# Optimization experiments

Hardware: AMD Instinct MI355X
Metric: run time of the kernel (lower is better)

Reference implementation:

```python
import jax, jax.numpy as jnp
import numpy as np

N, D, C, E, K = 100000, 64, 40, 1600000, 2

def setup_inputs() -> dict:
    key = jax.random.key(0)
    k1, k2, k3 = jax.random.split(key, 3)
    x = jax.random.normal(k1, (N, D), dtype=jnp.float32)
    edge_index = jax.random.randint(k2, (2, E), 0, N, dtype=jnp.int64)
    W = jax.random.normal(k3, (D, C), dtype=jnp.float32) * 0.05
    b = jnp.zeros((C,), dtype=jnp.float32)
    return {"x": x, "edge_index": edge_index, "W": W, "b": b}

def reference(x, edge_index, W, b):
    n = x.shape[0]
    self_loop = jnp.arange(n, dtype=edge_index.dtype)
    row = jnp.concatenate([edge_index[0], self_loop])  # [E+N]
    col = jnp.concatenate([edge_index[1], self_loop])  # [E+N]
    # degree over row (out-degree incl. self loops), as in torch_geometric.utils.degree
    deg = jax.ops.segment_sum(jnp.ones_like(row, dtype=x.dtype), row, num_segments=n)
    deg_inv_sqrt = jnp.where(deg > 0, jax.lax.rsqrt(deg), 0.0)
    norm = deg_inv_sqrt[row] * deg_inv_sqrt[col]  # [E+N]
    # K hops of SpMM: out[r] += norm_e * x[c] for each edge e=(r,c)
    for _ in range(K):
        x = jax.ops.segment_sum(norm[:, None] * x[col], row, num_segments=n)
    logits = x @ W + b  # [N, C]
    return jax.nn.log_softmax(logits, axis=1)
```

## Files before the change

kernel.cpp:

```cpp
#include <hip/hip_runtime.h>
#include <math.h>


#define D_FEAT 64
#define NCLS 40
#define BROWS 512
#define BROWS_LOG 9
#define BINCAP 10240
#define CSRCAP 12288
#define EPT 25

typedef float v2f __attribute__((ext_vector_type(2)));

__device__ __forceinline__ unsigned pack_bf16_2(float lo, float hi) {
    unsigned ulo = __float_as_uint(lo);
    unsigned uhi = __float_as_uint(hi);
    ulo = (ulo + 0x7fffu + ((ulo >> 16) & 1u)) >> 16;
    uhi = (uhi + 0x7fffu + ((uhi >> 16) & 1u)) & 0xffff0000u;
    return uhi | ulo;
}

__device__ __forceinline__ void acc2p(unsigned u, v2f& a) {
    v2f v;
    v.x = __uint_as_float(u << 16);
    v.y = __uint_as_float(u & 0xffff0000u);
    a += v;
}

__global__ void zero_cursors_kernel(int* __restrict__ cur, int nb) {
    int i = blockIdx.x * blockDim.x + threadIdx.x;
    if (i < nb) cur[i] = 0;
}

__global__ __launch_bounds__(256) void bin_edges_kernel(const int* __restrict__ rows,
                                                        const int* __restrict__ cols,
                                                        int* __restrict__ bucket_cursor,
                                                        unsigned* __restrict__ bins,
                                                        int e, int nb) {
    __shared__ int cnt[512];
    for (int i = threadIdx.x; i < nb; i += 256) cnt[i] = 0;
    __syncthreads();
    int base = blockIdx.x * (256 * EPT) + threadIdx.x;
    int rr[EPT], cc[EPT];
#pragma unroll
    for (int k = 0; k < EPT; k++) {
        int idx = base + k * 256;
        if (idx < e) { rr[k] = rows[idx]; cc[k] = cols[idx]; }
        else { rr[k] = -1; cc[k] = 0; }
    }
#pragma unroll
    for (int k = 0; k < EPT; k++)
        if (rr[k] >= 0) atomicAdd(&cnt[rr[k] >> BROWS_LOG], 1);
    __syncthreads();
    for (int i = threadIdx.x; i < nb; i += 256) {
        int c = cnt[i];
        cnt[i] = (c > 0) ? atomicAdd(&bucket_cursor[i], c) : 0;
    }
    __syncthreads();
#pragma unroll
    for (int k = 0; k < EPT; k++) {
        if (rr[k] >= 0) {
            int b = rr[k] >> BROWS_LOG;
            int pos = atomicAdd(&cnt[b], 1);
            bins[(size_t)b * BINCAP + pos] =
                ((unsigned)(rr[k] & (BROWS - 1)) << 17) | (unsigned)cc[k];
        }
    }
}

__global__ __launch_bounds__(512) void build_csr_kernel(const unsigned* __restrict__ bins,
                                                        const int* __restrict__ bucket_cursor,
                                                        int* __restrict__ csr_col,
                                                        uint2* __restrict__ row_info,
                                                        float* __restrict__ dis,
                                                        int* __restrict__ perm, int n) {
    __shared__ int cnt[512];
    __shared__ int sm[512];
    __shared__ int cur[512];
    __shared__ int lcsr[CSRCAP];
    int b = blockIdx.x;
    int tid = threadIdx.x;
    int m = bucket_cursor[b];
    cnt[tid] = 0;
    __syncthreads();
    const unsigned* bp = bins + (size_t)b * BINCAP;
    for (int i = tid; i < m; i += 512) atomicAdd(&cnt[bp[i] >> 17], 1);
    __syncthreads();
    int c = cnt[tid];
    int padded = (c + 3) & ~3;
    int r = b * BROWS + tid;
    if (r < n) dis[r] = rsqrtf(1.0f + (float)c);
    sm[tid] = padded;
    __syncthreads();
    for (int off = 1; off < 512; off <<= 1) {
        int t = (tid >= off) ? sm[tid - off] : 0;
        __syncthreads();
        sm[tid] += t;
        __syncthreads();
    }
    int off0 = sm[tid] - padded;
    cur[tid] = off0;
    if (r < n) row_info[r] = make_uint2((unsigned)(b * CSRCAP + off0), (unsigned)padded);
    __syncthreads();
    for (int i = tid; i < m; i += 512) {
        unsigned u = bp[i];
        int pos = atomicAdd(&cur[u >> 17], 1);
        lcsr[pos] = (int)(u & 0x1FFFFu);
    }
    __syncthreads();
    if (r < n) {
        for (int j = c; j < padded; j++) lcsr[off0 + j] = n;
    }
    __syncthreads();
    int tot = sm[511];
    int4* cp4 = (int4*)(csr_col + (size_t)b * CSRCAP);
    const int4* l4 = (const int4*)lcsr;
    for (int i = tid; i < (tot >> 2); i += 512) cp4[i] = l4[i];

    __syncthreads();
    if (tid < 64) cnt[tid] = 0;
    __syncthreads();
    int bin = min(padded >> 2, 63);
    if (r < n) atomicAdd(&cnt[bin], 1);
    __syncthreads();
    if (tid < 64) sm[tid] = cnt[tid];
    __syncthreads();
    for (int off = 1; off < 64; off <<= 1) {
        int t = (tid >= off && tid < 64) ? sm[tid - off] : 0;
        __syncthreads();
        if (tid < 64) sm[tid] += t;
        __syncthreads();
    }
    if (tid < 64) cur[tid] = sm[tid] - cnt[tid];
    __syncthreads();
    if (r < n) {
        int rank = atomicAdd(&cur[bin], 1);
        perm[b * BROWS + rank] = r;
    } else {
        perm[b * BROWS + tid] = -1;
    }
}

__global__ __launch_bounds__(256) void sort_rows_kernel(int* __restrict__ csr_col,
                                                        const uint2* __restrict__ row_info,
                                                        int n) {
    int wid = (int)((blockIdx.x * blockDim.x + threadIdx.x) >> 6);
    int lane = threadIdx.x & 63;
    int r0 = wid * 2, r1 = r0 + 1;
    if (r0 >= n) return;
    uint2 i0 = row_info[r0];
    uint2 i1 = (r1 < n) ? row_info[r1] : make_uint2(0u, 0u);
    int p0 = (int)i0.y, p1 = (int)i1.y;
    if (p0 <= 32 && p1 <= 32) {
        int half = lane >> 5, hl = lane & 31;
        int base = half ? (int)i1.x : (int)i0.x;
        int pad  = half ? p1 : p0;
        int key = (hl < pad) ? csr_col[base + hl] : 0x7fffffff;
#pragma unroll
        for (int k = 2; k <= 32; k <<= 1) {
#pragma unroll
            for (int j = k >> 1; j > 0; j >>= 1) {
                int other = __shfl_xor(key, j, 64);
                bool takeMin = (((hl & j) == 0) == ((hl & k) == 0));
                int mn = min(key, other), mx = max(key, other);
                key = takeMin ? mn : mx;
            }
        }
        if (hl < pad) csr_col[base + hl] = key;
    } else {
        for (int t = 0; t < 2; t++) {
            int base = t ? (int)i1.x : (int)i0.x;
            int pad  = t ? p1 : p0;
            if (pad == 0) continue;
            if (pad <= 64) {
                int key = (lane < pad) ? csr_col[base + lane] : 0x7fffffff;
#pragma unroll
                for (int k = 2; k <= 64; k <<= 1) {
#pragma unroll
                    for (int j = k >> 1; j > 0; j >>= 1) {
                        int other = __shfl_xor(key, j, 64);
                        bool takeMin = (((lane & j) == 0) == ((lane & k) == 0));
                        int mn = min(key, other), mx = max(key, other);
                        key = takeMin ? mn : mx;
                    }
                }
                if (lane < pad) csr_col[base + lane] = key;
            } else if (lane == 0) {
                for (int i2 = 1; i2 < pad; i2++) {
                    int kk = csr_col[base + i2];
                    int j2 = i2 - 1;
                    while (j2 >= 0 && csr_col[base + j2] > kk) {
                        csr_col[base + j2 + 1] = csr_col[base + j2]; j2--;
                    }
                    csr_col[base + j2 + 1] = kk;
                }
            }
        }
    }
}

__global__ void scale_x_kernel(const float* __restrict__ x, const float* __restrict__ dis,
                               unsigned* __restrict__ xs0, unsigned* __restrict__ xs1, int n) {
    int i = blockIdx.x * blockDim.x + threadIdx.x;
    int total = (n + 1) * (D_FEAT / 2);
    if (i >= total) return;
    int node = i >> 5;
    if (node < n) {
        float s = dis[node];
        float2 v = ((const float2*)x)[i];
        xs0[i] = pack_bf16_2(s * v.x, s * v.y);
    } else {
        xs0[i] = 0u;
        xs1[i] = 0u;
    }
}

#define GATHER16(cp, xs_in, ql, base, len)                                  \
    uint2 u0 = make_uint2(0u, 0u), u1 = u0, u2 = u0, u3 = u0;               \
    uint2 u4 = u0, u5 = u0, u6 = u0, u7 = u0;                               \
    uint2 u8 = u0, u9 = u0, u10 = u0, u11 = u0;                             \
    uint2 u12 = u0, u13 = u0, u14 = u0, u15 = u0;                           \
    if (base < len) {                                                       \
        uint4 cv = cp[(base >> 2) + 0];                                     \
        u0 = xs_in[cv.x * 16 + ql]; u1 = xs_in[cv.y * 16 + ql];             \
        u2 = xs_in[cv.z * 16 + ql]; u3 = xs_in[cv.w * 16 + ql];             \
    }                                                                       \
    if (base + 4 < len) {                                                   \
        uint4 cv = cp[(base >> 2) + 1];                                     \
        u4 = xs_in[cv.x * 16 + ql]; u5 = xs_in[cv.y * 16 + ql];             \
        u6 = xs_in[cv.z * 16 + ql]; u7 = xs_in[cv.w * 16 + ql];             \
    }                                                                       \
    if (base + 8 < len) {                                                   \
        uint4 cv = cp[(base >> 2) + 2];                                     \
        u8 = xs_in[cv.x * 16 + ql]; u9 = xs_in[cv.y * 16 + ql];             \
        u10 = xs_in[cv.z * 16 + ql]; u11 = xs_in[cv.w * 16 + ql];           \
    }                                                                       \
    if (base + 12 < len) {                                                  \
        uint4 cv = cp[(base >> 2) + 3];                                     \
        u12 = xs_in[cv.x * 16 + ql]; u13 = xs_in[cv.y * 16 + ql];           \
        u14 = xs_in[cv.z * 16 + ql]; u15 = xs_in[cv.w * 16 + ql];           \
    }                                                                       \
    acc2p(u0.x, h01); acc2p(u0.y, h23);                                     \
    acc2p(u1.x, h01); acc2p(u1.y, h23);                                     \
    acc2p(u2.x, h01); acc2p(u2.y, h23);                                     \
    acc2p(u3.x, h01); acc2p(u3.y, h23);                                     \
    acc2p(u4.x, h01); acc2p(u4.y, h23);                                     \
    acc2p(u5.x, h01); acc2p(u5.y, h23);                                     \
    acc2p(u6.x, h01); acc2p(u6.y, h23);                                     \
    acc2p(u7.x, h01); acc2p(u7.y, h23);                                     \
    acc2p(u8.x, h01); acc2p(u8.y, h23);                                     \
    acc2p(u9.x, h01); acc2p(u9.y, h23);                                     \
    acc2p(u10.x, h01); acc2p(u10.y, h23);                                   \
    acc2p(u11.x, h01); acc2p(u11.y, h23);                                   \
    acc2p(u12.x, h01); acc2p(u12.y, h23);                                   \
    acc2p(u13.x, h01); acc2p(u13.y, h23);                                   \
    acc2p(u14.x, h01); acc2p(u14.y, h23);                                   \
    acc2p(u15.x, h01); acc2p(u15.y, h23);

__global__ __launch_bounds__(256, 6) void spmm_hop1_kernel(const uint2* __restrict__ xs_in,
                                                           uint2* __restrict__ xs_out,
                                                           const int* __restrict__ perm,
                                                           const uint2* __restrict__ row_info,
                                                           const int* __restrict__ csr_col,
                                                           const float* __restrict__ dis,
                                                           int n, int nperm) {
    int wave = (blockIdx.x * blockDim.x + threadIdx.x) >> 6;
    int lane = threadIdx.x & 63;
    int q = lane >> 4, ql = lane & 15;
    int pidx = wave * 4 + q;
    int r = (pidx < nperm) ? perm[pidx] : -1;
    bool valid = (r >= 0);
    int s = 0, len = 0;
    if (valid) { uint2 info = row_info[r]; s = (int)info.x; len = (int)info.y; }
    int maxlen = len;
    maxlen = max(maxlen, __shfl_xor(maxlen, 16, 64));
    maxlen = max(maxlen, __shfl_xor(maxlen, 32, 64));

    v2f h01 = {0.f, 0.f}, h23 = {0.f, 0.f};
    const uint4* cp = (const uint4*)(csr_col + s);
    for (int base = 0; base < maxlen; base += 16) {
        GATHER16(cp, xs_in, ql, base, len)
    }
    if (valid) {
        uint2 us = xs_in[r * 16 + ql];
        acc2p(us.x, h01); acc2p(us.y, h23);
        float dr = dis[r];
        float dr2 = dr * dr;
        xs_out[r * 16 + ql] = make_uint2(pack_bf16_2(dr2 * h01.x, dr2 * h01.y),
                                         pack_bf16_2(dr2 * h23.x, dr2 * h23.y));
    }
}

__global__ __launch_bounds__(256, 6) void spmm_logits_kernel(const uint2* __restrict__ xs_in,
                                                             const int* __restrict__ perm,
                                                             const uint2* __restrict__ row_info,
                                                             const int* __restrict__ csr_col,
                                                             const float* __restrict__ dis,
                                                             const float* __restrict__ W,
                                                             const float* __restrict__ b,
                                                             float* __restrict__ out,
                                                             int n, int nperm) {
    __shared__ float Wt[NCLS][D_FEAT + 4];
    __shared__ float bl[NCLS];
    __shared__ float hl[16][D_FEAT + 4];
    for (int i = threadIdx.x; i < D_FEAT * NCLS; i += 256) {
        int d = i / NCLS, cc = i - d * NCLS;
        Wt[cc][d] = W[i];
    }
    for (int i = threadIdx.x; i < NCLS; i += 256) bl[i] = b[i];
    __syncthreads();

    int wave = (blockIdx.x * blockDim.x + threadIdx.x) >> 6;
    int lane = threadIdx.x & 63;
    int q = lane >> 4, ql = lane & 15;
    int pidx = wave * 4 + q;
    int r = (pidx < nperm) ? perm[pidx] : -1;
    bool valid = (r >= 0);
    int s = 0, len = 0;
    if (valid) { uint2 info = row_info[r]; s = (int)info.x; len = (int)info.y; }
    int maxlen = len;
    maxlen = max(maxlen, __shfl_xor(maxlen, 16, 64));
    maxlen = max(maxlen, __shfl_xor(maxlen, 32, 64));

    v2f h01 = {0.f, 0.f}, h23 = {0.f, 0.f};
    const uint4* cp = (const uint4*)(csr_col + s);
    for (int base = 0; base < maxlen; base += 16) {
        GATHER16(cp, xs_in, ql, base, len)
    }

    float y0, y1, y2;
    int c0 = ql, c1 = ql + 16;
    int c2 = (ql < 8) ? (ql + 32) : ql;
    {
        uint2 us = valid ? xs_in[r * 16 + ql] : make_uint2(0u, 0u);
        acc2p(us.x, h01); acc2p(us.y, h23);
        float dr = valid ? dis[r] : 0.f;
        float h0 = h01.x * dr, h1 = h01.y * dr, h2 = h23.x * dr, h3 = h23.y * dr;

        int rowslot = ((threadIdx.x >> 6) << 2) + q;
        *(float4*)&hl[rowslot][ql * 4] = make_float4(h0, h1, h2, h3);

        y0 = bl[c0]; y1 = bl[c1]; y2 = bl[c2];
#pragma unroll
        for (int g = 0; g < 16; g++) {
            float4 hv = *(const float4*)&hl[rowslot][g * 4];
            float4 w0 = *(const float4*)&Wt[c0][g * 4];
            float4 w1 = *(const float4*)&Wt[c1][g * 4];
            float4 w2 = *(const float4*)&Wt[c2][g * 4];
            y0 += hv.x * w0.x + hv.y * w0.y + hv.z * w0.z + hv.w * w0.w;
            y1 += hv.x * w1.x + hv.y * w1.y + hv.z * w1.z + hv.w * w1.w;
            y2 += hv.x * w2.x + hv.y * w2.y + hv.z * w2.z + hv.w * w2.w;
        }
    }

    bool has3 = (ql < 8);
    float m = fmaxf(y0, y1);
    if (has3) m = fmaxf(m, y2);
#pragma unroll
    for (int o = 8; o > 0; o >>= 1) m = fmaxf(m, __shfl_xor(m, o, 64));
    float sm = __expf(y0 - m) + __expf(y1 - m) + (has3 ? __expf(y2 - m) : 0.f);
#pragma unroll
    for (int o = 8; o > 0; o >>= 1) sm += __shfl_xor(sm, o, 64);
    float lse = m + __logf(sm);

    if (valid) {
        float* op = out + (long long)r * NCLS;
        op[ql] = y0 - lse;
        op[ql + 16] = y1 - lse;
        if (has3) op[ql + 32] = y2 - lse;
    }
}

extern "C" void kernel_launch(void* const* d_in, const int* in_sizes, int n_in,
                              void* d_out, int out_size, void* d_ws, size_t ws_size,
                              hipStream_t stream) {
    const float* x  = (const float*)d_in[0];
    const int*   ei = (const int*)d_in[1];
    const float* W  = (const float*)d_in[2];
    const float* b  = (const float*)d_in[3];
    float* out = (float*)d_out;

    const int n = in_sizes[0] / D_FEAT;
    const int e = in_sizes[1] / 2;
    const int nb = (n + BROWS - 1) / BROWS;

    const int* rows = ei;
    const int* cols = ei + e;

    size_t na = ((size_t)n + 256) & ~(size_t)255;
    size_t npm = (size_t)nb * BROWS;
    int*      bucket_cursor = (int*)d_ws;
    float*    dis           = (float*)(bucket_cursor + 256);
    uint2*    row_info      = (uint2*)(dis + na);
    int*      perm          = (int*)(row_info + na);
    unsigned* bins          = (unsigned*)(perm + npm);
    int*      csr_col       = (int*)(bins + (size_t)nb * BINCAP);
    unsigned* xs0           = (unsigned*)(csr_col + (size_t)nb * CSRCAP);
    unsigned* xs1           = xs0 + (size_t)(n + 1) * (D_FEAT / 2);

    const int BS = 256;

    zero_cursors_kernel<<<1, 256, 0, stream>>>(bucket_cursor, nb);
    {
        int blocks = (e + BS * EPT - 1) / (BS * EPT);
        bin_edges_kernel<<<blocks, BS, 0, stream>>>(rows, cols, bucket_cursor, bins, e, nb);
    }
    build_csr_kernel<<<nb, 512, 0, stream>>>(bins, bucket_cursor, csr_col, row_info, dis,
                                             perm, n);
    {
        int nwv = (n + 1) / 2;
        int blocks = (nwv * 64 + BS - 1) / BS;
        sort_rows_kernel<<<blocks, BS, 0, stream>>>(csr_col, row_info, n);
    }
    {
        int tot = (n + 1) * (D_FEAT / 2);
        scale_x_kernel<<<(tot + BS - 1) / BS, BS, 0, stream>>>(x, dis, xs0, xs1, n);
    }

    int nperm = (int)npm;
    int nwaves = nperm / 4;
    int blocks = (nwaves * 64 + BS - 1) / BS;
    spmm_hop1_kernel<<<blocks, BS, 0, stream>>>((const uint2*)xs0, (uint2*)xs1, perm,
                                                row_info, csr_col, dis, n, nperm);
    spmm_logits_kernel<<<blocks, BS, 0, stream>>>((const uint2*)xs1, perm, row_info, csr_col,
                                                  dis, W, b, out, n, nperm);
}
```

Measured before the change: 211.8 us.

## Widen SpMM gathers to 16-byte loads with 8 lanes per row, fuse sort and scale

The SpMM kernels now map 8 lanes per row, each loading a uint4 (8 bf16 features) instead of 16 lanes loading uint2, so each wave handles 8 rows. All 16 gathers are issued without predication (padded CSR tails now point to a zero row) behind a sched_barrier, and two accumulator sets split the dependency chain. Occupancy hint drops from 6 to 4. Separately, sort_rows and scale_x are fused into one launch, and the zero kernel is replaced by hipMemsetAsync. The aim is to cut gather instruction count and launch overhead, at the cost of more registers and unconditional loads past each row's length.

```diff
diff --git a/kernel.cpp b/kernel.cpp
--- a/kernel.cpp
+++ b/kernel.cpp
@@ -4,6 +4,7 @@
 
 #define D_FEAT 64
 #define NCLS 40
+#define D_PAD 72
 #define BROWS 512
 #define BROWS_LOG 9
 #define BINCAP 10240
@@ -25,11 +26,6 @@
     v.x = __uint_as_float(u << 16);
     v.y = __uint_as_float(u & 0xffff0000u);
     a += v;
-}
-
-__global__ void zero_cursors_kernel(int* __restrict__ cur, int nb) {
-    int i = blockIdx.x * blockDim.x + threadIdx.x;
-    if (i < nb) cur[i] = 0;
 }
 
 __global__ __launch_bounds__(256) void bin_edges_kernel(const int* __restrict__ rows,
@@ -116,6 +112,10 @@
     int4* cp4 = (int4*)(csr_col + (size_t)b * CSRCAP);
     const int4* l4 = (const int4*)lcsr;
     for (int i = tid; i < (tot >> 2); i += 512) cp4[i] = l4[i];
+    {
+        int g = tot + tid;
+        if (g < CSRCAP) csr_col[(size_t)b * CSRCAP + g] = n;
+    }
 
     __syncthreads();
     if (tid < 64) cnt[tid] = 0;
@@ -141,10 +141,29 @@
     }
 }
 
-__global__ __launch_bounds__(256) void sort_rows_kernel(int* __restrict__ csr_col,
-                                                        const uint2* __restrict__ row_info,
-                                                        int n) {
-    int wid = (int)((blockIdx.x * blockDim.x + threadIdx.x) >> 6);
+__global__ __launch_bounds__(256) void sort_scale_kernel(int* __restrict__ csr_col,
+                                                         const uint2* __restrict__ row_info,
+                                                         const float* __restrict__ x,
+                                                         const float* __restrict__ dis,
+                                                         unsigned* __restrict__ xs0,
+                                                         unsigned* __restrict__ xs1,
+                                                         int n, int sortBlocks) {
+    if ((int)blockIdx.x >= sortBlocks) {
+        int i = ((int)blockIdx.x - sortBlocks) * 256 + threadIdx.x;
+        int total = (n + 1) * (D_FEAT / 2);
+        if (i >= total) return;
+        int node = i >> 5;
+        if (node < n) {
+            float s = dis[node];
+            float2 v = ((const float2*)x)[i];
+            xs0[i] = pack_bf16_2(s * v.x, s * v.y);
+        } else {
+            xs0[i] = 0u;
+            xs1[i] = 0u;
+        }
+        return;
+    }
+    int wid = ((int)blockIdx.x * 256 + (int)threadIdx.x) >> 6;
     int lane = threadIdx.x & 63;
     int r0 = wid * 2, r1 = r0 + 1;
     if (r0 >= n) return;
@@ -199,66 +218,30 @@
     }
 }
 
-__global__ void scale_x_kernel(const float* __restrict__ x, const float* __restrict__ dis,
-                               unsigned* __restrict__ xs0, unsigned* __restrict__ xs1, int n) {
-    int i = blockIdx.x * blockDim.x + threadIdx.x;
-    int total = (n + 1) * (D_FEAT / 2);
-    if (i >= total) return;
-    int node = i >> 5;
-    if (node < n) {
-        float s = dis[node];
-        float2 v = ((const float2*)x)[i];
-        xs0[i] = pack_bf16_2(s * v.x, s * v.y);
-    } else {
-        xs0[i] = 0u;
-        xs1[i] = 0u;
-    }
-}
-
-#define GATHER16(cp, xs_in, ql, base, len)                                  \
-    uint2 u0 = make_uint2(0u, 0u), u1 = u0, u2 = u0, u3 = u0;               \
-    uint2 u4 = u0, u5 = u0, u6 = u0, u7 = u0;                               \
-    uint2 u8 = u0, u9 = u0, u10 = u0, u11 = u0;                             \
-    uint2 u12 = u0, u13 = u0, u14 = u0, u15 = u0;                           \
-    if (base < len) {                                                       \
-        uint4 cv = cp[(base >> 2) + 0];                                     \
-        u0 = xs_in[cv.x * 16 + ql]; u1 = xs_in[cv.y * 16 + ql];             \
-        u2 = xs_in[cv.z * 16 + ql]; u3 = xs_in[cv.w * 16 + ql];             \
-    }                                                                       \
-    if (base + 4 < len) {                                                   \
-        uint4 cv = cp[(base >> 2) + 1];                                     \
-        u4 = xs_in[cv.x * 16 + ql]; u5 = xs_in[cv.y * 16 + ql];             \
-        u6 = xs_in[cv.z * 16 + ql]; u7 = xs_in[cv.w * 16 + ql];             \
-    }                                                                       \
-    if (base + 8 < len) {                                                   \
-        uint4 cv = cp[(base >> 2) + 2];                                     \
-        u8 = xs_in[cv.x * 16 + ql]; u9 = xs_in[cv.y * 16 + ql];             \
-        u10 = xs_in[cv.z * 16 + ql]; u11 = xs_in[cv.w * 16 + ql];           \
-    }                                                                       \
-    if (base + 12 < len) {                                                  \
-        uint4 cv = cp[(base >> 2) + 3];                                     \
-        u12 = xs_in[cv.x * 16 + ql]; u13 = xs_in[cv.y * 16 + ql];           \
-        u14 = xs_in[cv.z * 16 + ql]; u15 = xs_in[cv.w * 16 + ql];           \
-    }                                                                       \
-    acc2p(u0.x, h01); acc2p(u0.y, h23);                                     \
-    acc2p(u1.x, h01); acc2p(u1.y, h23);                                     \
-    acc2p(u2.x, h01); acc2p(u2.y, h23);                                     \
-    acc2p(u3.x, h01); acc2p(u3.y, h23);                                     \
-    acc2p(u4.x, h01); acc2p(u4.y, h23);                                     \
-    acc2p(u5.x, h01); acc2p(u5.y, h23);                                     \
-    acc2p(u6.x, h01); acc2p(u6.y, h23);                                     \
-    acc2p(u7.x, h01); acc2p(u7.y, h23);                                     \
-    acc2p(u8.x, h01); acc2p(u8.y, h23);                                     \
-    acc2p(u9.x, h01); acc2p(u9.y, h23);                                     \
-    acc2p(u10.x, h01); acc2p(u10.y, h23);                                   \
-    acc2p(u11.x, h01); acc2p(u11.y, h23);                                   \
-    acc2p(u12.x, h01); acc2p(u12.y, h23);                                   \
-    acc2p(u13.x, h01); acc2p(u13.y, h23);                                   \
-    acc2p(u14.x, h01); acc2p(u14.y, h23);                                   \
-    acc2p(u15.x, h01); acc2p(u15.y, h23);
-
-__global__ __launch_bounds__(256, 6) void spmm_hop1_kernel(const uint2* __restrict__ xs_in,
-                                                           uint2* __restrict__ xs_out,
+#define ACC4A(u) acc2p(u.x, hA01); acc2p(u.y, hA23); acc2p(u.z, hA45); acc2p(u.w, hA67);
+#define ACC4B(u) acc2p(u.x, hB01); acc2p(u.y, hB23); acc2p(u.z, hB45); acc2p(u.w, hB67);
+
+#define GATHER16_U4(cp, xs4, el, base, len)                                 \
+    uint4 cv0 = cp[(base >> 2) + 0];                                        \
+    uint4 cv1 = cp[(base >> 2) + 1];                                        \
+    uint4 cv2 = cp[(base >> 2) + 2];                                        \
+    uint4 cv3 = cp[(base >> 2) + 3];                                        \
+    uint4 u0 = xs4[cv0.x * 8 + el], u1 = xs4[cv0.y * 8 + el];               \
+    uint4 u2 = xs4[cv0.z * 8 + el], u3 = xs4[cv0.w * 8 + el];               \
+    uint4 u4 = xs4[cv1.x * 8 + el], u5 = xs4[cv1.y * 8 + el];               \
+    uint4 u6 = xs4[cv1.z * 8 + el], u7 = xs4[cv1.w * 8 + el];               \
+    uint4 u8 = xs4[cv2.x * 8 + el], u9 = xs4[cv2.y * 8 + el];               \
+    uint4 u10 = xs4[cv2.z * 8 + el], u11 = xs4[cv2.w * 8 + el];             \
+    uint4 u12 = xs4[cv3.x * 8 + el], u13 = xs4[cv3.y * 8 + el];             \
+    uint4 u14 = xs4[cv3.z * 8 + el], u15 = xs4[cv3.w * 8 + el];             \
+    __builtin_amdgcn_sched_barrier(0);                                      \
+    if (base < len)      { ACC4A(u0)  ACC4A(u1)  ACC4A(u2)  ACC4A(u3)  }    \
+    if (base + 4 < len)  { ACC4B(u4)  ACC4B(u5)  ACC4B(u6)  ACC4B(u7)  }    \
+    if (base + 8 < len)  { ACC4A(u8)  ACC4A(u9)  ACC4A(u10) ACC4A(u11) }    \
+    if (base + 12 < len) { ACC4B(u12) ACC4B(u13) ACC4B(u14) ACC4B(u15) }
+
+__global__ __launch_bounds__(256, 4) void spmm_hop1_kernel(const uint4* __restrict__ xs_in,
+                                                           uint4* __restrict__ xs_out,
                                                            const int* __restrict__ perm,
                                                            const uint2* __restrict__ row_info,
                                                            const int* __restrict__ csr_col,
@@ -266,32 +249,38 @@
                                                            int n, int nperm) {
     int wave = (blockIdx.x * blockDim.x + threadIdx.x) >> 6;
     int lane = threadIdx.x & 63;
-    int q = lane >> 4, ql = lane & 15;
-    int pidx = wave * 4 + q;
+    int e = lane >> 3, el = lane & 7;
+    int pidx = wave * 8 + e;
     int r = (pidx < nperm) ? perm[pidx] : -1;
     bool valid = (r >= 0);
     int s = 0, len = 0;
     if (valid) { uint2 info = row_info[r]; s = (int)info.x; len = (int)info.y; }
     int maxlen = len;
+    maxlen = max(maxlen, __shfl_xor(maxlen, 8, 64));
     maxlen = max(maxlen, __shfl_xor(maxlen, 16, 64));
     maxlen = max(maxlen, __shfl_xor(maxlen, 32, 64));
 
-    v2f h01 = {0.f, 0.f}, h23 = {0.f, 0.f};
+    v2f hA01 = {0.f,0.f}, hA23 = {0.f,0.f}, hA45 = {0.f,0.f}, hA67 = {0.f,0.f};
+    v2f hB01 = {0.f,0.f}, hB23 = {0.f,0.f}, hB45 = {0.f,0.f}, hB67 = {0.f,0.f};
     const uint4* cp = (const uint4*)(csr_col + s);
     for (int base = 0; base < maxlen; base += 16) {
-        GATHER16(cp, xs_in, ql, base, len)
+        GATHER16_U4(cp, xs_in, el, base, len)
     }
     if (valid) {
-        uint2 us = xs_in[r * 16 + ql];
-        acc2p(us.x, h01); acc2p(us.y, h23);
+        v2f h01 = hA01 + hB01, h23 = hA23 + hB23;
+        v2f h45 = hA45 + hB45, h67 = hA67 + hB67;
+        uint4 us = xs_in[r * 8 + el];
+        acc2p(us.x, h01); acc2p(us.y, h23); acc2p(us.z, h45); acc2p(us.w, h67);
         float dr = dis[r];
-        float dr2 = dr * dr;
-        xs_out[r * 16 + ql] = make_uint2(pack_bf16_2(dr2 * h01.x, dr2 * h01.y),
-                                         pack_bf16_2(dr2 * h23.x, dr2 * h23.y));
-    }
-}
-
-__global__ __launch_bounds__(256, 6) void spmm_logits_kernel(const uint2* __restrict__ xs_in,
+        float d2 = dr * dr;
+        xs_out[r * 8 + el] = make_uint4(pack_bf16_2(d2 * h01.x, d2 * h01.y),
+                                        pack_bf16_2(d2 * h23.x, d2 * h23.y),
+                                        pack_bf16_2(d2 * h45.x, d2 * h45.y),
+                                        pack_bf16_2(d2 * h67.x, d2 * h67.y));
+    }
+}
+
+__global__ __launch_bounds__(256, 4) void spmm_logits_kernel(const uint4* __restrict__ xs_in,
                                                              const int* __restrict__ perm,
                                                              const uint2* __restrict__ row_info,
                                                              const int* __restrict__ csr_col,
@@ -300,9 +289,9 @@
                                                              const float* __restrict__ b,
                                                              float* __restrict__ out,
                                                              int n, int nperm) {
-    __shared__ float Wt[NCLS][D_FEAT + 4];
+    __shared__ float Wt[NCLS][D_PAD];
     __shared__ float bl[NCLS];
-    __shared__ float hl[16][D_FEAT + 4];
+    __shared__ float hl[32][D_PAD];
     for (int i = threadIdx.x; i < D_FEAT * NCLS; i += 256) {
         int d = i / NCLS, cc = i - d * NCLS;
         Wt[cc][d] = W[i];
@@ -312,62 +301,72 @@
 
     int wave = (blockIdx.x * blockDim.x + threadIdx.x) >> 6;
     int lane = threadIdx.x & 63;
-    int q = lane >> 4, ql = lane & 15;
-    int pidx = wave * 4 + q;
+    int e = lane >> 3, el = lane & 7;
+    int pidx = wave * 8 + e;
     int r = (pidx < nperm) ? perm[pidx] : -1;
     bool valid = (r >= 0);
     int s = 0, len = 0;
     if (valid) { uint2 info = row_info[r]; s = (int)info.x; len = (int)info.y; }
     int maxlen = len;
+    maxlen = max(maxlen, __shfl_xor(maxlen, 8, 64));
     maxlen = max(maxlen, __shfl_xor(maxlen, 16, 64));
     maxlen = max(maxlen, __shfl_xor(maxlen, 32, 64));
 
-    v2f h01 = {0.f, 0.f}, h23 = {0.f, 0.f};
+    v2f hA01 = {0.f,0.f}, hA23 = {0.f,0.f}, hA45 = {0.f,0.f}, hA67 = {0.f,0.f};
+    v2f hB01 = {0.f,0.f}, hB23 = {0.f,0.f}, hB45 = {0.f,0.f}, hB67 = {0.f,0.f};
     const uint4* cp = (const uint4*)(csr_col + s);
     for (int base = 0; base < maxlen; base += 16) {
-        GATHER16(cp, xs_in, ql, base, len)
-    }
-
-    float y0, y1, y2;
-    int c0 = ql, c1 = ql + 16;
-    int c2 = (ql < 8) ? (ql + 32) : ql;
+        GATHER16_U4(cp, xs_in, el, base, len)
+    }
+
+    int rs = ((threadIdx.x >> 6) << 3) + e;
+    float y0, y1, y2, y3, y4;
+    int c0 = el, c1 = el + 8, c2 = el + 16, c3 = el + 24, c4 = el + 32;
     {
-        uint2 us = valid ? xs_in[r * 16 + ql] : make_uint2(0u, 0u);
-        acc2p(us.x, h01); acc2p(us.y, h23);
+        v2f h01 = hA01 + hB01, h23 = hA23 + hB23;
+        v2f h45 = hA45 + hB45, h67 = hA67 + hB67;
+        uint4 us = valid ? xs_in[r * 8 + el] : make_uint4(0u, 0u, 0u, 0u);
+        acc2p(us.x, h01); acc2p(us.y, h23); acc2p(us.z, h45); acc2p(us.w, h67);
         float dr = valid ? dis[r] : 0.f;
-        float h0 = h01.x * dr, h1 = h01.y * dr, h2 = h23.x * dr, h3 = h23.y * dr;
-
-        int rowslot = ((threadIdx.x >> 6) << 2) + q;
-        *(float4*)&hl[rowslot][ql * 4] = make_float4(h0, h1, h2, h3);
-
-        y0 = bl[c0]; y1 = bl[c1]; y2 = bl[c2];
+
+        *(float4*)&hl[rs][el * 8] =
+            make_float4(h01.x * dr, h01.y * dr, h23.x * dr, h23.y * dr);
+        *(float4*)&hl[rs][el * 8 + 4] =
+            make_float4(h45.x * dr, h45.y * dr, h67.x * dr, h67.y * dr);
+
+        y0 = bl[c0]; y1 = bl[c1]; y2 = bl[c2]; y3 = bl[c3]; y4 = bl[c4];
 #pragma unroll
         for (int g = 0; g < 16; g++) {
-            float4 hv = *(const float4*)&hl[rowslot][g * 4];
+            float4 hv = *(const float4*)&hl[rs][g * 4];
             float4 w0 = *(const float4*)&Wt[c0][g * 4];
             float4 w1 = *(const float4*)&Wt[c1][g * 4];
             float4 w2 = *(const float4*)&Wt[c2][g * 4];
+            float4 w3 = *(const float4*)&Wt[c3][g * 4];
+            float4 w4 = *(const float4*)&Wt[c4][g * 4];
             y0 += hv.x * w0.x + hv.y * w0.y + hv.z * w0.z + hv.w * w0.w;
             y1 += hv.x * w1.x + hv.y * w1.y + hv.z * w1.z + hv.w * w1.w;
             y2 += hv.x * w2.x + hv.y * w2.y + hv.z * w2.z + hv.w * w2.w;
+            y3 += hv.x * w3.x + hv.y * w3.y + hv.z * w3.z + hv.w * w3.w;
+            y4 += hv.x * w4.x + hv.y * w4.y + hv.z * w4.z + hv.w * w4.w;
         }
     }
 
-    bool has3 = (ql < 8);
-    float m = fmaxf(y0, y1);
-    if (has3) m = fmaxf(m, y2);
-#pragma unroll
-    for (int o = 8; o > 0; o >>= 1) m = fmaxf(m, __shfl_xor(m, o, 64));
-    float sm = __expf(y0 - m) + __expf(y1 - m) + (has3 ? __expf(y2 - m) : 0.f);
-#pragma unroll
-    for (int o = 8; o > 0; o >>= 1) sm += __shfl_xor(sm, o, 64);
+    float m = fmaxf(fmaxf(fmaxf(y0, y1), fmaxf(y2, y3)), y4);
+#pragma unroll
+    for (int o = 4; o > 0; o >>= 1) m = fmaxf(m, __shfl_xor(m, o, 64));
+    float sm = __expf(y0 - m) + __expf(y1 - m) + __expf(y2 - m) +
+               __expf(y3 - m) + __expf(y4 - m);
+#pragma unroll
+    for (int o = 4; o > 0; o >>= 1) sm += __shfl_xor(sm, o, 64);
     float lse = m + __logf(sm);
 
     if (valid) {
         float* op = out + (long long)r * NCLS;
-        op[ql] = y0 - lse;
-        op[ql + 16] = y1 - lse;
-        if (has3) op[ql + 32] = y2 - lse;
+        op[c0] = y0 - lse;
+        op[c1] = y1 - lse;
+        op[c2] = y2 - lse;
+        op[c3] = y3 - lse;
+        op[c4] = y4 - lse;
     }
 }
 
@@ -400,7 +399,7 @@
 
     const int BS = 256;
 
-    zero_cursors_kernel<<<1, 256, 0, stream>>>(bucket_cursor, nb);
+    hipMemsetAsync(bucket_cursor, 0, (size_t)nb * sizeof(int), stream);
     {
         int blocks = (e + BS * EPT - 1) / (BS * EPT);
         bin_edges_kernel<<<blocks, BS, 0, stream>>>(rows, cols, bucket_cursor, bins, e, nb);
@@ -409,19 +408,18 @@
                                              perm, n);
     {
         int nwv = (n + 1) / 2;
-        int blocks = (nwv * 64 + BS - 1) / BS;
-        sort_rows_kernel<<<blocks, BS, 0, stream>>>(csr_col, row_info, n);
-    }
-    {
+        int sortBlocks = (nwv * 64 + BS - 1) / BS;
         int tot = (n + 1) * (D_FEAT / 2);
-        scale_x_kernel<<<(tot + BS - 1) / BS, BS, 0, stream>>>(x, dis, xs0, xs1, n);
+        int scaleBlocks = (tot + BS - 1) / BS;
+        sort_scale_kernel<<<sortBlocks + scaleBlocks, BS, 0, stream>>>(
+            csr_col, row_info, x, dis, xs0, xs1, n, sortBlocks);
     }
 
     int nperm = (int)npm;
-    int nwaves = nperm / 4;
+    int nwaves = nperm / 8;
     int blocks = (nwaves * 64 + BS - 1) / BS;
-    spmm_hop1_kernel<<<blocks, BS, 0, stream>>>((const uint2*)xs0, (uint2*)xs1, perm,
+    spmm_hop1_kernel<<<blocks, BS, 0, stream>>>((const uint4*)xs0, (uint4*)xs1, perm,
                                                 row_info, csr_col, dis, n, nperm);
-    spmm_logits_kernel<<<blocks, BS, 0, stream>>>((const uint2*)xs1, perm, row_info, csr_col,
+    spmm_logits_kernel<<<blocks, BS, 0, stream>>>((const uint4*)xs1, perm, row_info, csr_col,
                                                   dis, W, b, out, n, nperm);
 }
```

After: 207.4 us. -2.1%, faster.
